# Optimization experiments

Measured on AMD Instinct MI355X. Metric: run time of the kernel, lower is better.

## Reference

```python
import jax, jax.numpy as jnp
import numpy as np

NUM_HEADS = 12
DIM = 768
HEAD_DIM = DIM // NUM_HEADS
SCALE = HEAD_DIM ** -0.5
LORA_ALPHA = 1.0


def setup_inputs() -> dict:
    key = jax.random.key(0)
    ks = jax.random.split(key, 9)
    B, H, W = 1, 64, 64
    return {
        "x": jax.random.normal(ks[0], (B, H, W, DIM), jnp.float32),
        "w_qkv": jax.random.normal(ks[1], (3 * DIM, DIM), jnp.float32) * 0.02,
        "b_qkv": jax.random.normal(ks[2], (3 * DIM,), jnp.float32) * 0.02,
        "lora_A": jax.random.normal(ks[3], (12, DIM), jnp.float32) * 0.02,
        "lora_B": jax.random.normal(ks[4], (3 * DIM, 12), jnp.float32) * 0.02,
        "w_proj": jax.random.normal(ks[5], (DIM, DIM), jnp.float32) * 0.02,
        "b_proj": jax.random.normal(ks[6], (DIM,), jnp.float32) * 0.02,
        "rel_pos_h": jax.random.normal(ks[7], (2 * H - 1, HEAD_DIM), jnp.float32) * 0.02,
        "rel_pos_w": jax.random.normal(ks[8], (2 * W - 1, HEAD_DIM), jnp.float32) * 0.02,
    }


def _get_rel_pos(size: int, rel_pos: jnp.ndarray) -> jnp.ndarray:
    # q_size == k_size and rel_pos.shape[0] == 2*size-1, so no interpolation.
    coords = jnp.arange(size)[:, None] - jnp.arange(size)[None, :] + (size - 1)
    return rel_pos[coords]  # [size, size, head_dim]


def reference(x, w_qkv, b_qkv, lora_A, lora_B, w_proj, b_proj, rel_pos_h, rel_pos_w):
    B, H, W, _ = x.shape
    N = H * W
    # LoRA qkv projection: W_eff path = base + alpha * x @ (B A)^T
    qkv = x @ w_qkv.T + b_qkv + LORA_ALPHA * ((x @ lora_A.T) @ lora_B.T)
    qkv = qkv.reshape(B, N, 3, NUM_HEADS, HEAD_DIM)
    qkv = jnp.transpose(qkv, (2, 0, 3, 1, 4)).reshape(3, B * NUM_HEADS, N, HEAD_DIM)
    q, k, v = qkv[0], qkv[1], qkv[2]
    attn = jnp.einsum('bqc,bkc->bqk', q * SCALE, k)  # [B*nh, N, N]
    # decomposed relative position bias
    Rh = _get_rel_pos(H, rel_pos_h)  # [H, H, hd]
    Rw = _get_rel_pos(W, rel_pos_w)  # [W, W, hd]
    r_q = q.reshape(B * NUM_HEADS, H, W, HEAD_DIM)
    rel_h = jnp.einsum('bhwc,hkc->bhwk', r_q, Rh)
    rel_w = jnp.einsum('bhwc,wkc->bhwk', r_q, Rw)
    attn = (attn.reshape(-1, H, W, H, W)
            + rel_h[:, :, :, :, None]
            + rel_w[:, :, :, None, :]).reshape(-1, N, N)
    attn = jax.nn.softmax(attn, axis=-1)
    out = jnp.einsum('bqk,bkc->bqc', attn, v)  # [B*nh, N, hd]
    out = out.reshape(B, NUM_HEADS, H, W, HEAD_DIM)
    out = jnp.transpose(out, (0, 2, 3, 1, 4)).reshape(B, H, W, DIM)
    return out @ w_proj.T + b_proj
```

## Files before the change

### kernel.cpp

```cpp
#include <hip/hip_runtime.h>
#include <stdint.h>


typedef __attribute__((ext_vector_type(4))) float f32x4;
typedef __attribute__((ext_vector_type(16))) float f32x16;
typedef __attribute__((ext_vector_type(4))) float fvec4;
typedef __attribute__((ext_vector_type(8))) short s16x8;
typedef __attribute__((ext_vector_type(4))) short s16x4;
typedef __attribute__((ext_vector_type(4))) unsigned u32x4;

constexpr int NH  = 12;
constexpr int HD  = 64;
constexpr int DIM = 768;
constexpr int N   = 4096;
constexpr int QKV = 2304;
constexpr float LOG2E  = 1.4426950408889634f;
constexpr float SCALE2 = 0.125f * LOG2E;

static __device__ __forceinline__ short f2bf(float f) {
  unsigned u = __builtin_bit_cast(unsigned, f);
  unsigned r = (u + 0x7FFFu + ((u >> 16) & 1u)) >> 16;
  return (short)r;
}
static __device__ __forceinline__ float bf2f(short s) {
  unsigned u = ((unsigned)(unsigned short)s) << 16;
  return __builtin_bit_cast(float, u);
}
static __device__ __forceinline__ unsigned cvt_pk_bf16(float a, float b) {
  unsigned r;
  asm("v_cvt_pk_bf16_f32 %0, %1, %2" : "=v"(r) : "v"(a), "v"(b));
  return r;
}
static __device__ __forceinline__ float ex2(float x) {
  float r;
  asm("v_exp_f32 %0, %1" : "=v"(r) : "v"(x));
  return r;
}
static __device__ __forceinline__ void gload16(const void* g, void* l) {
  __builtin_amdgcn_global_load_lds(
      (const __attribute__((address_space(1))) void*)g,
      (__attribute__((address_space(3))) void*)l, 16, 0, 0);
}
static __device__ __forceinline__ void barrier_pre() {
  __builtin_amdgcn_s_barrier();
  __builtin_amdgcn_sched_barrier(0);
}
static __device__ __forceinline__ void barrier_post() {
  __builtin_amdgcn_sched_barrier(0);
  __builtin_amdgcn_s_barrier();
  __builtin_amdgcn_sched_barrier(0);
}

__global__ __launch_bounds__(256) void k_weff(const float* __restrict__ w_qkv,
                                              const float* __restrict__ lora_A,
                                              const float* __restrict__ lora_B,
                                              short* __restrict__ weff) {
  int e = blockIdx.x * 256 + threadIdx.x;
  if (e >= QKV * DIM) return;
  int r = e / DIM, c = e % DIM;
  float acc = w_qkv[e];
#pragma unroll
  for (int t = 0; t < 12; ++t) acc += lora_B[r * 12 + t] * lora_A[t * DIM + c];
  weff[e] = f2bf(acc);
}

__global__ __launch_bounds__(256) void k_x2bf(const float* __restrict__ x,
                                              short* __restrict__ xb) {
  int i = blockIdx.x * 256 + threadIdx.x;
  fvec4 v = *reinterpret_cast<const fvec4*>(x + (size_t)i * 4);
  s16x4 p;
  p[0] = f2bf(v[0]); p[1] = f2bf(v[1]); p[2] = f2bf(v[2]); p[3] = f2bf(v[3]);
  *reinterpret_cast<s16x4*>(xb + (size_t)i * 4) = p;
}

__global__ __launch_bounds__(256) void k_wsplit(const float* __restrict__ w,
                                                short* __restrict__ ws) {
  int r = blockIdx.y;
  int kk = blockIdx.x * 256 + threadIdx.x;
  int blk = (kk >= 1536) ? 2 : (kk >= 768 ? 1 : 0);
  int c = kk - blk * 768;
  float wv = w[(size_t)r * 768 + c];
  short hi = f2bf(wv);
  ws[(size_t)r * 2304 + kk] = (blk == 1) ? f2bf(wv - bf2f(hi)) : hi;
}

template <int KIT, int MODE, int BM>
__global__ __launch_bounds__(256, 2) void k_gemm(const short* __restrict__ A,
                                                 const short* __restrict__ B,
                                                 const float* __restrict__ bias,
                                                 short* __restrict__ qo,
                                                 short* __restrict__ ko,
                                                 short* __restrict__ vo,
                                                 float* __restrict__ outf) {
  constexpr int MFR = BM / 32;
  constexpr int BUFB = BM * 128 + 16384;
  __shared__ __align__(16) char lds[2 * BUFB];
  const int tid = threadIdx.x;
  const int wave = tid >> 6, lane = tid & 63, lr = lane & 15, lg = lane >> 4;
  const int wr = wave >> 1, wc = wave & 1;
  const int i0 = blockIdx.x * BM, j0 = blockIdx.y * 128;
  const int LDA = KIT * 128;

  size_t offA[MFR], offB[4];
#pragma unroll
  for (int it = 0; it < MFR; ++it) {
    int c = it * 256 + tid;
    int row = c >> 3;
    offA[it] = (size_t)row * LDA + (((c & 7) << 4) ^ ((row & 7) << 4));
  }
#pragma unroll
  for (int it = 0; it < 4; ++it) {
    int c = it * 256 + tid;
    int row = c >> 3;
    offB[it] = (size_t)row * LDA + (((c & 7) << 4) ^ ((row & 7) << 4));
  }
  const char* Ab = (const char*)A + (size_t)i0 * LDA;
  const char* Bb = (const char*)B + (size_t)j0 * LDA;

  auto STAGE = [&](int kt, int b) {
    char* base = lds + b * BUFB;
    const size_t kadd = (size_t)kt * 128;
#pragma unroll
    for (int it = 0; it < MFR; ++it)
      gload16(Ab + kadd + offA[it], base + wave * 1024 + it * 4096);
#pragma unroll
    for (int it = 0; it < 4; ++it)
      gload16(Bb + kadd + offB[it], base + BM * 128 + wave * 1024 + it * 4096);
  };

  const int swz = (lr & 7) << 4;
  const int ab = (wr * (BM / 2) + lr) * 128 + ((lg * 16) ^ swz);
  const int bb = BM * 128 + (wc * 64 + lr) * 128 + ((lg * 16) ^ swz);

  f32x4 acc[MFR][4] = {};

  STAGE(0, 0);
  for (int kt = 0; kt < KIT; ++kt) {
    const int buf = kt & 1;
    if (kt + 1 < KIT) {
      STAGE(kt + 1, buf ^ 1);
      if constexpr (BM == 128)
        asm volatile("s_waitcnt vmcnt(8)" ::: "memory");
      else
        asm volatile("s_waitcnt vmcnt(6)" ::: "memory");
    } else {
      asm volatile("s_waitcnt vmcnt(0)" ::: "memory");
    }
    barrier_pre();
    const char* bufp = lds + buf * BUFB;
#pragma unroll
    for (int ks2 = 0; ks2 < 2; ++ks2) {
      s16x8 af[MFR], bf_[4];
#pragma unroll
      for (int m = 0; m < MFR; ++m)
        af[m] = *reinterpret_cast<const s16x8*>(bufp + ((ab + m * 2048) ^ (ks2 << 6)));
#pragma unroll
      for (int n = 0; n < 4; ++n)
        bf_[n] = *reinterpret_cast<const s16x8*>(bufp + ((bb + n * 2048) ^ (ks2 << 6)));
#pragma unroll
      for (int m = 0; m < MFR; ++m)
#pragma unroll
        for (int n = 0; n < 4; ++n)
          acc[m][n] = __builtin_amdgcn_mfma_f32_16x16x32_bf16(af[m], bf_[n], acc[m][n], 0, 0, 0);
    }
    barrier_post();
  }

  if constexpr (MODE == 0) {
    const int three = j0 / 768;
    const int head = ((j0 % 768) >> 6) + wc;
    short* dst = (three == 0) ? qo : ((three == 1) ? ko : vo);
#pragma unroll
    for (int n = 0; n < 4; ++n) {
      const int col = n * 16 + lr;
      const float bj = bias[j0 + wc * 64 + col];
#pragma unroll
      for (int m = 0; m < MFR; ++m)
#pragma unroll
        for (int r = 0; r < 4; ++r) {
          int i = i0 + wr * (BM / 2) + m * 16 + lg * 4 + r;
          dst[((size_t)head * N + i) * HD + col] = f2bf(acc[m][n][r] + bj);
        }
    }
  } else {
#pragma unroll
    for (int n = 0; n < 4; ++n) {
      const int j = j0 + wc * 64 + n * 16 + lr;
      const float bj = bias[j];
#pragma unroll
      for (int m = 0; m < MFR; ++m)
#pragma unroll
        for (int r = 0; r < 4; ++r) {
          int i = i0 + wr * (BM / 2) + m * 16 + lg * 4 + r;
          outf[(size_t)i * 768 + j] = acc[m][n][r] + bj;
        }
    }
  }
}

__global__ __launch_bounds__(256) void k_vT(const short* __restrict__ vg,
                                            short* __restrict__ vTg) {
  __shared__ short ts[64 * 72];
  const int tid = threadIdx.x;
  const int i0 = blockIdx.x * 64;
  const int h = blockIdx.y;
#pragma unroll
  for (int it = 0; it < 2; ++it) {
    int ch = tid + 256 * it;
    int row = ch >> 3, cc = (ch & 7) * 8;
    *reinterpret_cast<s16x8*>(&ts[row * 72 + cc]) =
        *reinterpret_cast<const s16x8*>(&vg[((size_t)h * N + i0 + row) * HD + cc]);
  }
  __syncthreads();
#pragma unroll
  for (int it = 0; it < 2; ++it) {
    int ch = tid + 256 * it;
    int c = ch >> 3, ii = (ch & 7) * 8;
    s16x8 o;
#pragma unroll
    for (int j = 0; j < 8; ++j) o[j] = ts[(ii + j) * 72 + c];
    *reinterpret_cast<s16x8*>(&vTg[((size_t)h * HD + c) * N + i0 + ii]) = o;
  }
}

__global__ __launch_bounds__(256) void k_relh(const short* __restrict__ qg,
                                              const float* __restrict__ tab,
                                              short* __restrict__ rhT) {
  __shared__ short Ts[64 * 72];
  const int tid = threadIdx.x;
  const int wave = tid >> 6, lane = tid & 63, lr = lane & 15, lg = lane >> 4;
  const int h = blockIdx.x >> 6, qh = blockIdx.x & 63;
#pragma unroll
  for (int it = 0; it < 4; ++it) {
    int e = tid + 256 * it;
    int row = e >> 4, c4 = (e & 15) * 4;
    fvec4 v = *reinterpret_cast<const fvec4*>(tab + (size_t)(qh + 63 - row) * 64 + c4);
    s16x4 p;
    p[0] = f2bf(v[0]); p[1] = f2bf(v[1]); p[2] = f2bf(v[2]); p[3] = f2bf(v[3]);
    *reinterpret_cast<s16x4*>(&Ts[row * 72 + c4]) = p;
  }
  __syncthreads();
  const size_t qrow = (size_t)h * N + qh * 64 + wave * 16 + lr;
  const s16x8 a0 = *reinterpret_cast<const s16x8*>(qg + qrow * 64 + lg * 8);
  const s16x8 a1 = *reinterpret_cast<const s16x8*>(qg + qrow * 64 + 32 + lg * 8);
  f32x4 acc[4] = {};
#pragma unroll
  for (int ks2 = 0; ks2 < 2; ++ks2)
#pragma unroll
    for (int n = 0; n < 4; ++n) {
      s16x8 b = *reinterpret_cast<const s16x8*>(&Ts[(n * 16 + lr) * 72 + ks2 * 32 + lg * 8]);
      acc[n] = __builtin_amdgcn_mfma_f32_16x16x32_bf16(ks2 ? a1 : a0, b, acc[n], 0, 0, 0);
    }
  const size_t ob = ((size_t)(h * 64 + qh)) * 4096;
#pragma unroll
  for (int n = 0; n < 4; ++n) {
    s16x4 o;
#pragma unroll
    for (int r = 0; r < 4; ++r) o[r] = f2bf(acc[n][r]);
    *reinterpret_cast<s16x4*>(&rhT[ob + (size_t)(n * 16 + lr) * 64 + wave * 16 + lg * 4]) = o;
  }
}

__global__ __launch_bounds__(256) void k_relw(const short* __restrict__ qg,
                                              const float* __restrict__ tab,
                                              short* __restrict__ rwg) {
  __shared__ short Ts[128 * 72];
  const int tid = threadIdx.x;
  const int wave = tid >> 6, lane = tid & 63, lr = lane & 15, lg = lane >> 4;
  const int h = blockIdx.x >> 6, qh = blockIdx.x & 63;
#pragma unroll
  for (int it = 0; it < 8; ++it) {
    int e = tid + 256 * it;
    int row = e >> 4, c4 = (e & 15) * 4;
    s16x4 p = {0, 0, 0, 0};
    if (row < 127) {
      fvec4 v = *reinterpret_cast<const fvec4*>(tab + (size_t)row * 64 + c4);
      p[0] = f2bf(v[0]); p[1] = f2bf(v[1]); p[2] = f2bf(v[2]); p[3] = f2bf(v[3]);
    }
    *reinterpret_cast<s16x4*>(&Ts[row * 72 + c4]) = p;
  }
  __syncthreads();
  const size_t qrow = (size_t)h * N + qh * 64 + wave * 16 + lr;
  const s16x8 a0 = *reinterpret_cast<const s16x8*>(qg + qrow * 64 + lg * 8);
  const s16x8 a1 = *reinterpret_cast<const s16x8*>(qg + qrow * 64 + 32 + lg * 8);
  f32x4 acc[8] = {};
#pragma unroll
  for (int ks2 = 0; ks2 < 2; ++ks2)
#pragma unroll
    for (int n = 0; n < 8; ++n) {
      s16x8 b = *reinterpret_cast<const s16x8*>(&Ts[(n * 16 + lr) * 72 + ks2 * 32 + lg * 8]);
      acc[n] = __builtin_amdgcn_mfma_f32_16x16x32_bf16(ks2 ? a1 : a0, b, acc[n], 0, 0, 0);
    }
  const size_t ob = ((size_t)h * N + qh * 64) * 64;
#pragma unroll
  for (int n = 0; n < 8; ++n) {
    int d = n * 16 + lr;
#pragma unroll
    for (int r = 0; r < 4; ++r) {
      int qw = wave * 16 + lg * 4 + r;
      int kw = qw + 63 - d;
      if ((unsigned)kw < 64u) rwg[ob + (size_t)qw * 64 + kw] = f2bf(acc[n][r]);
    }
  }
}

#define QG_BLOCK(QB0, QB1, QB2, QB3, RW, RH2, ACC0, ACC1, LA, LB)              \
  do {                                                                         \
    f32x16 sa = {};                                                            \
    __builtin_amdgcn_s_setprio(1);                                             \
    sa = __builtin_amdgcn_mfma_f32_32x32x16_bf16(kf0, QB0, sa, 0, 0, 0);       \
    sa = __builtin_amdgcn_mfma_f32_32x32x16_bf16(kf1, QB1, sa, 0, 0, 0);       \
    sa = __builtin_amdgcn_mfma_f32_32x32x16_bf16(kf2, QB2, sa, 0, 0, 0);       \
    sa = __builtin_amdgcn_mfma_f32_32x32x16_bf16(kf3, QB3, sa, 0, 0, 0);       \
    __builtin_amdgcn_s_setprio(0);                                             \
    float p[16];                                                               \
    _Pragma("unroll")                                                          \
    for (int reg = 0; reg < 16; ++reg)                                         \
      p[reg] = ex2(fmaf(sa[reg], SCALE2, RH2 + RW[reg]));                      \
    float t0 = (p[0] + p[1]) + (p[2] + p[3]);                                  \
    float t1 = (p[4] + p[5]) + (p[6] + p[7]);                                  \
    float t2 = (p[8] + p[9]) + (p[10] + p[11]);                                \
    float t3 = (p[12] + p[13]) + (p[14] + p[15]);                              \
    LA += t0 + t1;                                                             \
    LB += t2 + t3;                                                             \
    unsigned w00 = cvt_pk_bf16(p[0], p[1]),   w01 = cvt_pk_bf16(p[2], p[3]);   \
    unsigned w10 = cvt_pk_bf16(p[4], p[5]),   w11 = cvt_pk_bf16(p[6], p[7]);   \
    unsigned w20 = cvt_pk_bf16(p[8], p[9]),   w21 = cvt_pk_bf16(p[10], p[11]); \
    unsigned w30 = cvt_pk_bf16(p[12], p[13]), w31 = cvt_pk_bf16(p[14], p[15]); \
    asm("v_permlane32_swap_b32 %0, %1" : "+v"(w00), "+v"(w10));                \
    asm("v_permlane32_swap_b32 %0, %1" : "+v"(w01), "+v"(w11));                \
    asm("v_permlane32_swap_b32 %0, %1" : "+v"(w20), "+v"(w30));                \
    asm("v_permlane32_swap_b32 %0, %1" : "+v"(w21), "+v"(w31));                \
    u32x4 u0 = {w00, w01, w10, w11};                                           \
    u32x4 u1 = {w20, w21, w30, w31};                                           \
    s16x8 pa0 = __builtin_bit_cast(s16x8, u0);                                 \
    s16x8 pa1 = __builtin_bit_cast(s16x8, u1);                                 \
    __builtin_amdgcn_s_setprio(1);                                             \
    ACC0 = __builtin_amdgcn_mfma_f32_32x32x16_bf16(pa0, vf0, ACC0, 0, 0, 0);   \
    ACC0 = __builtin_amdgcn_mfma_f32_32x32x16_bf16(pa1, vf2, ACC0, 0, 0, 0);   \
    ACC1 = __builtin_amdgcn_mfma_f32_32x32x16_bf16(pa0, vf1, ACC1, 0, 0, 0);   \
    ACC1 = __builtin_amdgcn_mfma_f32_32x32x16_bf16(pa1, vf3, ACC1, 0, 0, 0);   \
    __builtin_amdgcn_s_setprio(0);                                             \
  } while (0)

#define FLASH_BODY(BUFOFF, RHU0, RHU1)                                         \
  do {                                                                         \
    const char* bufp = lds + (BUFOFF);                                         \
    s16x8 kf0 = *reinterpret_cast<const s16x8*>(bufp + kco0);                  \
    s16x8 kf1 = *reinterpret_cast<const s16x8*>(bufp + kco1);                  \
    s16x8 kf2 = *reinterpret_cast<const s16x8*>(bufp + kco2);                  \
    s16x8 kf3 = *reinterpret_cast<const s16x8*>(bufp + kco3);                  \
    s16x8 vf0 = *reinterpret_cast<const s16x8*>(bufp + vco0);                  \
    s16x8 vf1 = *reinterpret_cast<const s16x8*>(bufp + vco1);                  \
    s16x8 vf2 = *reinterpret_cast<const s16x8*>(bufp + vco2);                  \
    s16x8 vf3 = *reinterpret_cast<const s16x8*>(bufp + vco3);                  \
    const float rh20 = LOG2E * bf2f((short)(RHU0));                            \
    const float rh21 = LOG2E * bf2f((short)(RHU1));                            \
    QG_BLOCK(qb00, qb01, qb02, qb03, rw0, rh20, acc00, acc01, la0, lb0);       \
    QG_BLOCK(qb10, qb11, qb12, qb13, rw1, rh21, acc10, acc11, la1, lb1);       \
  } while (0)

__global__ __launch_bounds__(256, 2) void k_flash(const short* __restrict__ qg,
                                                  const short* __restrict__ kg,
                                                  const short* __restrict__ vTg,
                                                  const short* __restrict__ rhTg,
                                                  const short* __restrict__ rwg,
                                                  short* __restrict__ aprime) {
  __shared__ __align__(16) char lds[65536];
  const int tid = threadIdx.x;
  const int wave = tid >> 6, lane = tid & 63;
  const int ql = lane & 31, hi = lane >> 5;
  const int kt2 = wave & 1, kh2 = wave >> 1;
  const int bid = blockIdx.x;
  const int id = (bid & 7) * 96 + (bid >> 3);
  const int h = id >> 6, qt = id & 63;
  const int i0 = qt * 64;

  const short* q0p = qg + ((size_t)h * N + i0 + ql) * 64 + hi * 8;
  const short* q1p = q0p + 32 * 64;
  const s16x8 qb00 = *reinterpret_cast<const s16x8*>(q0p);
  const s16x8 qb01 = *reinterpret_cast<const s16x8*>(q0p + 16);
  const s16x8 qb02 = *reinterpret_cast<const s16x8*>(q0p + 32);
  const s16x8 qb03 = *reinterpret_cast<const s16x8*>(q0p + 48);
  const s16x8 qb10 = *reinterpret_cast<const s16x8*>(q1p);
  const s16x8 qb11 = *reinterpret_cast<const s16x8*>(q1p + 16);
  const s16x8 qb12 = *reinterpret_cast<const s16x8*>(q1p + 32);
  const s16x8 qb13 = *reinterpret_cast<const s16x8*>(q1p + 48);

  f32x16 rw0, rw1;
  {
    const short* rwp0 = rwg + ((size_t)h * N + i0 + ql) * 64 + kh2 * 32 + hi * 4;
    const short* rwp1 = rwp0 + 32 * 64;
#pragma unroll
    for (int reg = 0; reg < 16; ++reg) {
      int o = (reg & 3) + 8 * (reg >> 2);
      rw0[reg] = LOG2E * bf2f(rwp0[o]);
      rw1[reg] = LOG2E * bf2f(rwp1[o]);
    }
  }
  const short* rhp = rhTg + ((size_t)(h * 64 + qt)) * 4096;

  int soff[8];
  const char* sbase;
  if (wave < 2) {
    sbase = (const char*)kg + (size_t)h * N * 128 + wave * 64 * 128;
#pragma unroll
    for (int it = 0; it < 8; ++it) {
      int c = it * 64 + lane, row = c >> 3;
      soff[it] = row * 128 + (((c & 7) << 4) ^ ((row & 7) << 4));
    }
  } else {
    sbase = (const char*)vTg + (size_t)h * 64 * 8192 + (wave - 2) * 128;
#pragma unroll
    for (int it = 0; it < 8; ++it) {
      int c = it * 64 + lane, r = c >> 3;
      soff[it] = r * 8192 + (((c & 7) << 4) ^ ((r & 7) << 4));
    }
  }
  const int sstep = (wave < 2) ? 16384 : 256;
  char* lreg = lds + wave * 8192;

  auto STAGE = [&](int i, int buf) {
    const char* sp = sbase + (size_t)i * sstep;
    char* lp = lreg + buf * 32768;
#pragma unroll
    for (int it = 0; it < 8; ++it) gload16(sp + soff[it], lp + it * 1024);
  };

  const int swzq = (ql & 7) << 4;
  const int krow = (kt2 * 64 + kh2 * 32 + ql) * 128;
  const int kco0 = krow + ((0 * 32 + hi * 16) ^ swzq);
  const int kco1 = krow + ((1 * 32 + hi * 16) ^ swzq);
  const int kco2 = krow + ((2 * 32 + hi * 16) ^ swzq);
  const int kco3 = krow + ((3 * 32 + hi * 16) ^ swzq);
  const int vrow0 = 16384 + kt2 * 8192 + ql * 128;
  const int vrow1 = vrow0 + 32 * 128;
  const int vch0 = (kh2 * 64 + 0 * 32 + hi * 16) ^ swzq;
  const int vch1 = (kh2 * 64 + 1 * 32 + hi * 16) ^ swzq;
  const int vco0 = vrow0 + vch0;
  const int vco1 = vrow1 + vch0;
  const int vco2 = vrow0 + vch1;
  const int vco3 = vrow1 + vch1;

  f32x16 acc00 = {}, acc01 = {}, acc10 = {}, acc11 = {};
  float la0 = 0.f, lb0 = 0.f, la1 = 0.f, lb1 = 0.f;

  STAGE(0, 0);
  unsigned short rA0 = (unsigned short)rhp[(size_t)kt2 * 64 + ql];
  unsigned short rA1 = (unsigned short)rhp[(size_t)kt2 * 64 + 32 + ql];
  unsigned short rB0 = 0, rB1 = 0;

  for (int ii = 0; ii < 16; ++ii) {
    const int i = 2 * ii;
    STAGE(i + 1, 1);
    rB0 = (unsigned short)rhp[(size_t)((i + 1) * 2 + kt2) * 64 + ql];
    rB1 = (unsigned short)rhp[(size_t)((i + 1) * 2 + kt2) * 64 + 32 + ql];
    asm volatile("s_waitcnt vmcnt(10)" ::: "memory");
    barrier_pre();
    FLASH_BODY(0, rA0, rA1);
    barrier_post();
    if (i + 2 < 32) {
      STAGE(i + 2, 0);
      rA0 = (unsigned short)rhp[(size_t)((i + 2) * 2 + kt2) * 64 + ql];
      rA1 = (unsigned short)rhp[(size_t)((i + 2) * 2 + kt2) * 64 + 32 + ql];
      asm volatile("s_waitcnt vmcnt(10)" ::: "memory");
    } else {
      asm volatile("s_waitcnt vmcnt(0)" ::: "memory");
    }
    barrier_pre();
    FLASH_BODY(32768, rB0, rB1);
    barrier_post();
  }

  float l0 = la0 + lb0, l1 = la1 + lb1;
  l0 += __shfl_xor(l0, 32);
  l1 += __shfl_xor(l1, 32);
  float* LS = (float*)lds;
  if (lane < 32) {
    LS[wave * 64 + ql] = l0;
    LS[wave * 64 + 32 + ql] = l1;
  }
  __syncthreads();
  const int eq = wave * 16 + (lane >> 2);
  const int cb = (lane & 3) * 16;
  float inv = 1.0f / (LS[eq] + LS[64 + eq] + LS[128 + eq] + LS[192 + eq]);
  __syncthreads();
  float* OF = (float*)lds;
#pragma unroll
  for (int qg2 = 0; qg2 < 2; ++qg2)
#pragma unroll
    for (int ct = 0; ct < 2; ++ct) {
      const f32x16& a = qg2 ? (ct ? acc11 : acc10) : (ct ? acc01 : acc00);
#pragma unroll
      for (int reg = 0; reg < 16; ++reg) {
        int q = qg2 * 32 + (reg & 3) + 8 * (reg >> 2) + 4 * hi;
        int c = ct * 32 + ql;
        OF[wave * 4096 + q * 64 + (c ^ ((q & 7) << 2))] = a[reg];
      }
    }
  __syncthreads();
  f32x4 osum[4] = {};
#pragma unroll
  for (int w = 0; w < 4; ++w)
#pragma unroll
    for (int j = 0; j < 4; ++j)
      osum[j] += *reinterpret_cast<const f32x4*>(
          &OF[w * 4096 + eq * 64 + ((cb + j * 4) ^ ((eq & 7) << 2))]);

  s16x8 hi8[2], lo8[2];
#pragma unroll
  for (int j = 0; j < 4; ++j)
#pragma unroll
    for (int e = 0; e < 4; ++e) {
      float o = osum[j][e] * inv;
      short oh = f2bf(o);
      float lo = o - bf2f(oh);
      int idx = j * 4 + e;
      hi8[idx >> 3][idx & 7] = oh;
      lo8[idx >> 3][idx & 7] = f2bf(lo);
    }
  size_t obase = (size_t)(i0 + eq) * 2304 + h * 64 + cb;
  *reinterpret_cast<s16x8*>(&aprime[obase]) = hi8[0];
  *reinterpret_cast<s16x8*>(&aprime[obase + 8]) = hi8[1];
  *reinterpret_cast<s16x8*>(&aprime[obase + 768]) = hi8[0];
  *reinterpret_cast<s16x8*>(&aprime[obase + 776]) = hi8[1];
  *reinterpret_cast<s16x8*>(&aprime[obase + 1536]) = lo8[0];
  *reinterpret_cast<s16x8*>(&aprime[obase + 1544]) = lo8[1];
}

extern "C" void kernel_launch(void* const* d_in, const int* in_sizes, int n_in,
                              void* d_out, int out_size, void* d_ws, size_t ws_size,
                              hipStream_t stream) {
  const float* x      = (const float*)d_in[0];
  const float* w_qkv  = (const float*)d_in[1];
  const float* b_qkv  = (const float*)d_in[2];
  const float* lora_A = (const float*)d_in[3];
  const float* lora_B = (const float*)d_in[4];
  const float* w_proj = (const float*)d_in[5];
  const float* b_proj = (const float*)d_in[6];
  const float* rel_h  = (const float*)d_in[7];
  const float* rel_w  = (const float*)d_in[8];
  float* out = (float*)d_out;

  char* ws = (char*)d_ws;
  short* weff   = (short*)(ws + 0);
  short* xb     = (short*)(ws + 3538944);
  short* vg     = (short*)(ws + 9830400);
  short* aprime = (short*)(ws + 0);
  short* qg     = (short*)(ws + 18874368);
  short* kg     = (short*)(ws + 25165824);
  short* vTg    = (short*)(ws + 31457280);
  short* rhT    = (short*)(ws + 37748736);
  short* rwg    = (short*)(ws + 44040192);
  short* wsp    = (short*)(ws + 50331648);
  (void)ws_size; (void)in_sizes; (void)n_in; (void)out_size;

  k_weff<<<dim3((QKV * DIM + 255) / 256), dim3(256), 0, stream>>>(w_qkv, lora_A, lora_B, weff);
  k_x2bf<<<dim3(3072), dim3(256), 0, stream>>>(x, xb);
  k_wsplit<<<dim3(9, 768), dim3(256), 0, stream>>>(w_proj, wsp);
  k_gemm<12, 0, 128><<<dim3(32, 18), dim3(256), 0, stream>>>(xb, weff, b_qkv, qg, kg, vg, nullptr);
  k_vT<<<dim3(64, NH), dim3(256), 0, stream>>>(vg, vTg);
  k_relh<<<dim3(NH * 64), dim3(256), 0, stream>>>(qg, rel_h, rhT);
  k_relw<<<dim3(NH * 64), dim3(256), 0, stream>>>(qg, rel_w, rwg);
  k_flash<<<dim3(NH * 64), dim3(256), 0, stream>>>(qg, kg, vTg, rhT, rwg, aprime);
  k_gemm<36, 1, 64><<<dim3(64, 6), dim3(256), 0, stream>>>(aprime, wsp, b_proj, nullptr, nullptr, nullptr, out);
}
```

Baseline: 171.2 us.

## Stage per-wave private K/V tiles to drop block barriers in flash loop

```diff
diff --git a/kernel.cpp b/kernel.cpp
--- a/kernel.cpp
+++ b/kernel.cpp
@@ -345,7 +345,7 @@
 
 #define FLASH_BODY(BUFOFF, RHU0, RHU1)                                         \
   do {                                                                         \
-    const char* bufp = lds + (BUFOFF);                                         \
+    const char* bufp = wb + (BUFOFF);                                          \
     s16x8 kf0 = *reinterpret_cast<const s16x8*>(bufp + kco0);                  \
     s16x8 kf1 = *reinterpret_cast<const s16x8*>(bufp + kco1);                  \
     s16x8 kf2 = *reinterpret_cast<const s16x8*>(bufp + kco2);                  \
@@ -400,47 +400,43 @@
   }
   const short* rhp = rhTg + ((size_t)(h * 64 + qt)) * 4096;
 
-  int soff[8];
-  const char* sbase;
-  if (wave < 2) {
-    sbase = (const char*)kg + (size_t)h * N * 128 + wave * 64 * 128;
-#pragma unroll
-    for (int it = 0; it < 8; ++it) {
-      int c = it * 64 + lane, row = c >> 3;
-      soff[it] = row * 128 + (((c & 7) << 4) ^ ((row & 7) << 4));
-    }
-  } else {
-    sbase = (const char*)vTg + (size_t)h * 64 * 8192 + (wave - 2) * 128;
-#pragma unroll
-    for (int it = 0; it < 8; ++it) {
-      int c = it * 64 + lane, r = c >> 3;
-      soff[it] = r * 8192 + (((c & 7) << 4) ^ ((r & 7) << 4));
-    }
-  }
-  const int sstep = (wave < 2) ? 16384 : 256;
-  char* lreg = lds + wave * 8192;
+  const int kbrow = kt2 * 64 + kh2 * 32;
+  int koff[4], voff[4];
+#pragma unroll
+  for (int it = 0; it < 4; ++it) {
+    int c = it * 64 + lane;
+    int row = c >> 3, pos = c & 7, s = pos ^ (row & 7);
+    koff[it] = (kbrow + row) * 128 + s * 16;
+  }
+#pragma unroll
+  for (int it = 0; it < 4; ++it) {
+    int c = it * 64 + lane;
+    int r = c >> 3, pos = c & 7, s = pos ^ (r & 7);
+    voff[it] = (r + ((s >> 2) << 5)) * 8192 + (kbrow + ((s & 3) << 3)) * 2;
+  }
+  const char* kgb = (const char*)kg + (size_t)h * N * 128;
+  const char* vgb = (const char*)vTg + (size_t)h * 64 * 8192;
+  char* wb = lds + wave * 8192;
 
   auto STAGE = [&](int i, int buf) {
-    const char* sp = sbase + (size_t)i * sstep;
-    char* lp = lreg + buf * 32768;
-#pragma unroll
-    for (int it = 0; it < 8; ++it) gload16(sp + soff[it], lp + it * 1024);
+    const char* kp = kgb + (size_t)i * 16384;
+    const char* vp = vgb + (size_t)i * 256;
+    char* lp = wb + buf * 32768;
+#pragma unroll
+    for (int it = 0; it < 4; ++it) gload16(kp + koff[it], lp + it * 1024);
+#pragma unroll
+    for (int it = 0; it < 4; ++it) gload16(vp + voff[it], lp + 4096 + it * 1024);
   };
 
   const int swzq = (ql & 7) << 4;
-  const int krow = (kt2 * 64 + kh2 * 32 + ql) * 128;
-  const int kco0 = krow + ((0 * 32 + hi * 16) ^ swzq);
-  const int kco1 = krow + ((1 * 32 + hi * 16) ^ swzq);
-  const int kco2 = krow + ((2 * 32 + hi * 16) ^ swzq);
-  const int kco3 = krow + ((3 * 32 + hi * 16) ^ swzq);
-  const int vrow0 = 16384 + kt2 * 8192 + ql * 128;
-  const int vrow1 = vrow0 + 32 * 128;
-  const int vch0 = (kh2 * 64 + 0 * 32 + hi * 16) ^ swzq;
-  const int vch1 = (kh2 * 64 + 1 * 32 + hi * 16) ^ swzq;
-  const int vco0 = vrow0 + vch0;
-  const int vco1 = vrow1 + vch0;
-  const int vco2 = vrow0 + vch1;
-  const int vco3 = vrow1 + vch1;
+  const int kco0 = ql * 128 + ((0 * 32 + hi * 16) ^ swzq);
+  const int kco1 = ql * 128 + ((1 * 32 + hi * 16) ^ swzq);
+  const int kco2 = ql * 128 + ((2 * 32 + hi * 16) ^ swzq);
+  const int kco3 = ql * 128 + ((3 * 32 + hi * 16) ^ swzq);
+  const int vco0 = 4096 + ql * 128 + ((0 * 64 + 0 * 32 + hi * 16) ^ swzq);
+  const int vco1 = 4096 + ql * 128 + ((1 * 64 + 0 * 32 + hi * 16) ^ swzq);
+  const int vco2 = 4096 + ql * 128 + ((0 * 64 + 1 * 32 + hi * 16) ^ swzq);
+  const int vco3 = 4096 + ql * 128 + ((1 * 64 + 1 * 32 + hi * 16) ^ swzq);
 
   f32x16 acc00 = {}, acc01 = {}, acc10 = {}, acc11 = {};
   float la0 = 0.f, lb0 = 0.f, la1 = 0.f, lb1 = 0.f;
@@ -456,9 +452,8 @@
     rB0 = (unsigned short)rhp[(size_t)((i + 1) * 2 + kt2) * 64 + ql];
     rB1 = (unsigned short)rhp[(size_t)((i + 1) * 2 + kt2) * 64 + 32 + ql];
     asm volatile("s_waitcnt vmcnt(10)" ::: "memory");
-    barrier_pre();
+    __builtin_amdgcn_sched_barrier(0);
     FLASH_BODY(0, rA0, rA1);
-    barrier_post();
     if (i + 2 < 32) {
       STAGE(i + 2, 0);
       rA0 = (unsigned short)rhp[(size_t)((i + 2) * 2 + kt2) * 64 + ql];
@@ -467,11 +462,11 @@
     } else {
       asm volatile("s_waitcnt vmcnt(0)" ::: "memory");
     }
-    barrier_pre();
+    __builtin_amdgcn_sched_barrier(0);
     FLASH_BODY(32768, rB0, rB1);
-    barrier_post();
-  }
-
+  }
+
+  __syncthreads();
   float l0 = la0 + lb0, l1 = la1 + lb1;
   l0 += __shfl_xor(l0, 32);
   l1 += __shfl_xor(l1, 32);
```

Result: faster. 159.9 us (-6.6%).
